# Kernel tuning notes

Measured on AMD Instinct MI355X. Metric: run time of the kernel, lower is better.

## Reference

```python
import jax, jax.numpy as jnp
import numpy as np

B, C_IN, T = 32, 22, 5000
EMB, P = 64, 100
HOP, NFFT, SR = 25, 128, 250
MIN_SZ, MAX_SZ = 10, 100
OC = 40
SCALES = (9, 25, 49)
FC = OC * len(SCALES)
_freqs = np.arange(NFFT // 2 + 1) * SR / NFFT
MU_IDX = np.nonzero((_freqs >= 8) & (_freqs <= 13))[0]   # bins 5,6
BETA_IDX = np.nonzero((_freqs >= 13) & (_freqs <= 30))[0]  # bins 7..15


def setup_inputs() -> dict:
    key = jax.random.key(0)
    k = iter(jax.random.split(key, 16))
    inp = {"x": jax.random.normal(next(k), (B, C_IN, T), jnp.float32)}
    for i, s in enumerate(SCALES):
        inp[f"ms{i}_w1"] = jax.random.normal(next(k), (OC, 1, 1, s), jnp.float32) * 0.05
        inp[f"ms{i}_b1"] = jnp.zeros((OC,), jnp.float32)
        inp[f"ms{i}_w2"] = jax.random.normal(next(k), (OC, OC, C_IN, 1), jnp.float32) * 0.05
        inp[f"ms{i}_b2"] = jnp.zeros((OC,), jnp.float32)
        inp[f"ms{i}_g"] = jnp.ones((OC,), jnp.float32)
        inp[f"ms{i}_bt"] = jnp.zeros((OC,), jnp.float32)
        inp[f"ms{i}_m"] = jnp.zeros((OC,), jnp.float32)
        inp[f"ms{i}_v"] = jnp.ones((OC,), jnp.float32)
    inp["a_w1"] = jax.random.normal(next(k), (C_IN // 2, C_IN, 3), jnp.float32) * 0.05
    inp["a_b1"] = jnp.zeros((C_IN // 2,), jnp.float32)
    inp["a_g"] = jnp.ones((C_IN // 2,), jnp.float32)
    inp["a_bt"] = jnp.zeros((C_IN // 2,), jnp.float32)
    inp["a_m"] = jnp.zeros((C_IN // 2,), jnp.float32)
    inp["a_v"] = jnp.ones((C_IN // 2,), jnp.float32)
    inp["a_w2"] = jax.random.normal(next(k), (1, C_IN // 2, 1), jnp.float32) * 0.05
    inp["a_b2"] = jnp.zeros((1,), jnp.float32)
    inp["proj_w"] = jax.random.normal(next(k), (EMB, FC, 1), jnp.float32) * 0.05
    inp["proj_b"] = jnp.zeros((EMB,), jnp.float32)
    return inp


def _conv1d(x, w, pad):
    return jax.lax.conv_general_dilated(x, w, (1,), [(pad, pad)],
                                        dimension_numbers=("NCH", "OIH", "NCH"))


def _bn(y, g, bt, m, v):  # eval-mode BatchNorm over channel dim of [B, C, T]
    return (y - m[None, :, None]) * jax.lax.rsqrt(v[None, :, None] + 1e-5) * g[None, :, None] + bt[None, :, None]


def _branch(x, w1, b1, w2, b2, g, bt, m, v):
    # Conv2d(1,OC,(1,ks)) on [B,1,C,T] == per-channel 1D conv over time.
    oc, _, _, ks = w1.shape
    b_, c_, t_ = x.shape
    y = _conv1d(x.reshape(b_ * c_, 1, t_), w1.reshape(oc, 1, ks), (ks - 1) // 2) + b1[None, :, None]
    y = y.reshape(b_, c_, oc, t_).transpose(0, 2, 1, 3)            # [B, OC, C, T]
    # Conv2d(OC,OC,(C,1)) collapses the channel (height) dim.
    y = jnp.einsum("oih,biht->bot", w2[..., 0], y) + b2[None, :, None]
    return jax.nn.elu(_bn(y, g, bt, m, v))                         # [B, OC, T]


def _stft_power(x):
    # torchaudio Spectrogram: center=True, reflect pad, periodic hann, power=2
    pad = NFFT // 2
    xp = jnp.pad(x, ((0, 0), (0, 0), (pad, pad)), mode="reflect")
    nfr = T // HOP  # module truncates to t // hop frames
    idx = jnp.arange(nfr)[:, None] * HOP + jnp.arange(NFFT)[None, :]
    win = 0.5 * (1.0 - jnp.cos(2.0 * jnp.pi * jnp.arange(NFFT) / NFFT))
    frames = xp[..., idx] * win                                    # [B, C, nfr, NFFT]
    spec = jnp.fft.rfft(frames, axis=-1)
    return spec.real ** 2 + spec.imag ** 2                         # [B, C, nfr, NFFT//2+1]


def _interp_linear(a, n):  # F.interpolate(mode='linear', align_corners=False) on [B, L]
    L = a.shape[-1]
    pos = jnp.clip((jnp.arange(n) + 0.5) * (L / n) - 0.5, 0.0, L - 1.0)
    lo = jnp.floor(pos).astype(jnp.int32)
    hi = jnp.minimum(lo + 1, L - 1)
    w = pos - lo
    return a[:, lo] * (1.0 - w) + a[:, hi] * w


def _adaptive_grid(act):
    w = 1.0 / (act + 1e-6)
    w = w / jnp.sum(w, axis=1, keepdims=True)
    gs = jnp.clip(w * T, MIN_SZ, MAX_SZ)
    gs = gs * (T / jnp.sum(gs, axis=1, keepdims=True))
    gsr = jnp.round(gs).astype(jnp.int32)
    gsr = gsr.at[:, -1].add(T - jnp.sum(gsr, axis=1))
    gsf = jnp.clip(gsr, MIN_SZ, MAX_SZ)
    gsf = gsf.at[:, -1].add(T - jnp.sum(gsf, axis=1))
    return jnp.where(gsf < MIN_SZ, MIN_SZ, gsf)


def _forward(x, ms0_w1, ms0_b1, ms0_w2, ms0_b2, ms0_g, ms0_bt, ms0_m, ms0_v,
             ms1_w1, ms1_b1, ms1_w2, ms1_b2, ms1_g, ms1_bt, ms1_m, ms1_v,
             ms2_w1, ms2_b1, ms2_w2, ms2_b2, ms2_g, ms2_bt, ms2_m, ms2_v,
             a_w1, a_b1, a_g, a_bt, a_m, a_v, a_w2, a_b2, proj_w, proj_b):
    # ---- frequency-domain activity detector ----
    spec = _stft_power(x)                                          # [B, C, 200, F]
    comb = spec[..., MU_IDX].mean(-1) + spec[..., BETA_IDX].mean(-1)  # [B, C, 200]
    a = jax.nn.relu(_bn(_conv1d(comb, a_w1, 1) + a_b1[None, :, None], a_g, a_bt, a_m, a_v))
    a = jnp.einsum("oi,bit->bot", a_w2[..., 0], a)[:, 0] + a_b2[0]
    activity = jax.nn.sigmoid(a)                                   # [B, 200]
    act_i = _interp_linear(activity, P)                            # [B, P]
    grid = _adaptive_grid(act_i)                                   # [B, P] int32, sums ~= T
    ends = jnp.cumsum(grid, axis=1)
    starts = ends - grid
    # ---- multi-scale CNN features ----
    feats = jnp.concatenate([
        _branch(x, ms0_w1, ms0_b1, ms0_w2, ms0_b2, ms0_g, ms0_bt, ms0_m, ms0_v),
        _branch(x, ms1_w1, ms1_b1, ms1_w2, ms1_b2, ms1_g, ms1_bt, ms1_m, ms1_v),
        _branch(x, ms2_w1, ms2_b1, ms2_w2, ms2_b2, ms2_g, ms2_bt, ms2_m, ms2_v)],
        axis=1)                                                    # [B, FC, T]
    # ---- ragged per-patch avg+max pooling via segment reductions ----
    tix = jnp.arange(T)
    seg = jax.vmap(lambda e: jnp.searchsorted(e, tix, side="right"))(ends)  # [B,T] in [0,P]
    flat = (seg + jnp.arange(B)[:, None] * (P + 1)).reshape(-1)
    f = feats.transpose(0, 2, 1).reshape(B * T, FC)
    nseg = B * (P + 1)  # extra slot collects any overflow timesteps
    sums = jax.ops.segment_sum(f, flat, num_segments=nseg)
    cnt = jax.ops.segment_sum(jnp.ones((B * T, 1), f.dtype), flat, num_segments=nseg)
    mx = jax.ops.segment_max(f, flat, num_segments=nseg)
    avg = sums / jnp.maximum(cnt, 1.0)
    mx = jnp.where(cnt > 0, mx, 0.0)
    pooled = (avg + mx).reshape(B, P + 1, FC)[:, :P]               # combined avg+max
    valid = ((ends <= T) & (starts < ends))[..., None]
    pooled = jnp.where(valid, pooled, 0.0)
    emb = jnp.einsum("oc,bpc->bpo", proj_w[..., 0], pooled) + proj_b  # [B, P, EMB]
    return emb, grid, act_i


def reference(x, ms0_w1, ms0_b1, ms0_w2, ms0_b2, ms0_g, ms0_bt, ms0_m, ms0_v,
              ms1_w1, ms1_b1, ms1_w2, ms1_b2, ms1_g, ms1_bt, ms1_m, ms1_v,
              ms2_w1, ms2_b1, ms2_w2, ms2_b2, ms2_g, ms2_bt, ms2_m, ms2_v,
              a_w1, a_b1, a_g, a_bt, a_m, a_v, a_w2, a_b2, proj_w, proj_b):
    return _forward(x, ms0_w1, ms0_b1, ms0_w2, ms0_b2, ms0_g, ms0_bt, ms0_m, ms0_v,
                    ms1_w1, ms1_b1, ms1_w2, ms1_b2, ms1_g, ms1_bt, ms1_m, ms1_v,
                    ms2_w1, ms2_b1, ms2_w2, ms2_b2, ms2_g, ms2_bt, ms2_m, ms2_v,
                    a_w1, a_b1, a_g, a_bt, a_m, a_v, a_w2, a_b2, proj_w, proj_b)
```

## Files before the change

### kernel.cpp

```cpp
#include <hip/hip_runtime.h>
#include <hip/hip_bf16.h>
#include <math.h>
#include <string.h>

#define B 32
#define CIN 22
#define T 5000
#define EMB 64
#define P 100
#define HOP 25
#define OC 40
#define FC 120
#define NBIN 11
#define NFR 200

#define TCH 256
#define CROWS 304
#define RSTRIDE 40

#define XPAD 5128
#define TWROW 24

typedef unsigned short ushort_t;
typedef __attribute__((ext_vector_type(8))) short bf16x8;
typedef __attribute__((ext_vector_type(4))) float f32x4;

__device__ __forceinline__ unsigned short f2bf(float f) {
  unsigned u = __float_as_uint(f);
  unsigned r = (u + 0x7FFFu + ((u >> 16) & 1u)) >> 16;
  return (unsigned short)r;
}
__device__ __forceinline__ float bf2f(unsigned short u) {
  return __uint_as_float(((unsigned)u) << 16);
}
__device__ __forceinline__ float fast_elu(float y) {
  return y > 0.f ? y : (__builtin_amdgcn_exp2f(y * 1.44269504088896340736f) - 1.0f);
}
__device__ __forceinline__ unsigned pack2bf(float a, float b) {
  __hip_bfloat162 h = __float22bfloat162_rn(make_float2(a, b));
  unsigned u;
  memcpy(&u, &h, 4);
  return u;
}

struct SetupArgs {
  const float* w1[3]; const float* b1[3]; const float* w2[3]; const float* b2[3];
  const float* g[3];  const float* bt[3]; const float* m[3];  const float* v[3];
  unsigned short* pw;
  float* A; float* Bc; float* tw;
};

__global__ __launch_bounds__(256) void setup_all(SetupArgs args) {
  int bx = blockIdx.x;
  int tid = threadIdx.x;
  if (bx < 498) {
    int id = bx * 256 + tid;
    int s, KS, fbase, idl;
    if (id < 13824)       { s = 0; KS = 9;  fbase = 0;   idl = id; }
    else if (id < 52224)  { s = 1; KS = 25; fbase = 27;  idl = id - 13824; }
    else                  { s = 2; KS = 49; fbase = 102; idl = id - 52224; }
    int fi = idl >> 9, rem = idl & 511;
    int lane = rem >> 3, j = rem & 7;
    int k = fi / 3, ot = fi - k * 3;
    int m = lane & 15, h = ((lane >> 4) << 3) + j;
    int o = ot * 16 + m;
    float val = 0.f;
    if (h < CIN && o < OC) {
      const float* w1 = args.w1[s];
      const float* w2 = args.w2[s];
      for (int i = 0; i < OC; ++i)
        val = fmaf(w2[(o * OC + i) * CIN + h], w1[i * KS + k], val);
    }
    args.pw[(size_t)(fbase + fi) * 512 + rem] = f2bf(val);
  } else if (bx < 504) {
    int id = (bx - 498) * 256 + tid;
    if (id < 1408) {
      int n = id & 127, k = id >> 7;
      const double PI = 3.14159265358979323846;
      double ang = -2.0 * PI * (double)((k + 5) * n) / 128.0;
      double win = 0.5 * (1.0 - cos(2.0 * PI * (double)n / 128.0));
      args.tw[n * TWROW + 2 * k]     = (float)(cos(ang) * win);
      args.tw[n * TWROW + 2 * k + 1] = (float)(sin(ang) * win);
    } else if (id < 1536) {
      int n = id - 1408;
      args.tw[n * TWROW + 22] = 0.f;
      args.tw[n * TWROW + 23] = 0.f;
    }
  } else {
    if (tid < 120) {
      int s = tid / 40, o = tid - s * 40;
      const float* w2 = args.w2[s];
      float sc = args.g[s][o] / sqrtf(args.v[s][o] + 1e-5f);
      float cc = args.b2[s][o];
      for (int i = 0; i < OC; ++i) {
        float sh = 0.f;
        for (int h = 0; h < CIN; ++h) sh += w2[(o * OC + i) * CIN + h];
        cc = fmaf(args.b1[s][i], sh, cc);
      }
      args.A[tid] = sc;
      args.Bc[tid] = cc * sc + (args.bt[s][o] - args.m[s][o] * sc);
    }
  }
}

__global__ __launch_bounds__(256) void stft_comb(const float* __restrict__ x,
                                                 const float* __restrict__ tw,
                                                 float* __restrict__ comb) {
  __shared__ float xsh[XPAD];
  int bc = blockIdx.x;
  const float* xr = x + (size_t)bc * T;
  int tid = threadIdx.x;
  for (int i = tid; i < XPAD; i += 256) {
    int mm = i - 64;
    mm = (mm < 0) ? -mm : mm;
    mm = (mm >= T) ? (2 * T - 2 - mm) : mm;
    xsh[i] = xr[mm];
  }
  __syncthreads();
  int fr = tid;
  if (fr < NFR) {
    float cr[NBIN], ci[NBIN];
    #pragma unroll
    for (int k = 0; k < NBIN; ++k) { cr[k] = 0.f; ci[k] = 0.f; }
    const float* xw = xsh + fr * HOP;
    #pragma unroll 2
    for (int n = 0; n < 128; ++n) {
      float xv = xw[n];
      const float4* t4 = reinterpret_cast<const float4*>(tw + n * TWROW);
      float4 w0 = t4[0], w1 = t4[1], w2 = t4[2], w3 = t4[3], w4 = t4[4], w5 = t4[5];
      cr[0] = fmaf(xv, w0.x, cr[0]); ci[0] = fmaf(xv, w0.y, ci[0]);
      cr[1] = fmaf(xv, w0.z, cr[1]); ci[1] = fmaf(xv, w0.w, ci[1]);
      cr[2] = fmaf(xv, w1.x, cr[2]); ci[2] = fmaf(xv, w1.y, ci[2]);
      cr[3] = fmaf(xv, w1.z, cr[3]); ci[3] = fmaf(xv, w1.w, ci[3]);
      cr[4] = fmaf(xv, w2.x, cr[4]); ci[4] = fmaf(xv, w2.y, ci[4]);
      cr[5] = fmaf(xv, w2.z, cr[5]); ci[5] = fmaf(xv, w2.w, ci[5]);
      cr[6] = fmaf(xv, w3.x, cr[6]); ci[6] = fmaf(xv, w3.y, ci[6]);
      cr[7] = fmaf(xv, w3.z, cr[7]); ci[7] = fmaf(xv, w3.w, ci[7]);
      cr[8] = fmaf(xv, w4.x, cr[8]); ci[8] = fmaf(xv, w4.y, ci[8]);
      cr[9] = fmaf(xv, w4.z, cr[9]); ci[9] = fmaf(xv, w4.w, ci[9]);
      cr[10] = fmaf(xv, w5.x, cr[10]); ci[10] = fmaf(xv, w5.y, ci[10]);
    }
    float p[NBIN];
    #pragma unroll
    for (int k = 0; k < NBIN; ++k) p[k] = cr[k] * cr[k] + ci[k] * ci[k];
    float beta = 0.f;
    #pragma unroll
    for (int k = 2; k < NBIN; ++k) beta += p[k];
    comb[bc * NFR + fr] = 0.5f * (p[0] + p[1]) + beta * (1.f / 9.f);
  }
}

__device__ __forceinline__ float wave_sum_f(float v) {
  #pragma unroll
  for (int off = 1; off < 64; off <<= 1) v += __shfl_xor(v, off);
  return v;
}
__device__ __forceinline__ int wave_sum_i(int v) {
  #pragma unroll
  for (int off = 1; off < 64; off <<= 1) v += __shfl_xor(v, off);
  return v;
}

struct MidSmem {
  union {
    struct {
      float cl[CIN * NFR];
      float actL[NFR];
      float aiL[P];
      float fL[P];
      int giL[P];
      int sI[P];
      float red;
    } a;
    unsigned short xs[CROWS * RSTRIDE];
  };
};

template <int KS, int FB, int SBASE>
__device__ __forceinline__ void scale_body(const unsigned short* __restrict__ xs,
                                           const unsigned short* __restrict__ pw,
                                           const float* __restrict__ Aff,
                                           const float* __restrict__ Bff,
                                           unsigned short* __restrict__ feats,
                                           int b, int t0, int wt0, int lane) {
  constexpr int PAD = (KS - 1) / 2;
  const int n = lane & 15, q = lane >> 4;
  f32x4 acc[3][4];
  #pragma unroll
  for (int ot = 0; ot < 3; ++ot)
    #pragma unroll
    for (int ti = 0; ti < 4; ++ti)
      acc[ot][ti] = (f32x4){0.f, 0.f, 0.f, 0.f};

  const unsigned short* pws = pw + (size_t)FB * 512 + lane * 8;
  #pragma unroll 1
  for (int k = 0; k < KS; ++k) {
    bf16x8 A0 = *(const bf16x8*)(pws + (size_t)(k * 3 + 0) * 512);
    bf16x8 A1 = *(const bf16x8*)(pws + (size_t)(k * 3 + 1) * 512);
    bf16x8 A2 = *(const bf16x8*)(pws + (size_t)(k * 3 + 2) * 512);
    int rbase = 24 - PAD + k + wt0 + n;
    #pragma unroll
    for (int ti = 0; ti < 4; ++ti) {
      bf16x8 Bf = *(const bf16x8*)(xs + (rbase + ti * 16) * RSTRIDE + q * 8);
      acc[0][ti] = __builtin_amdgcn_mfma_f32_16x16x32_bf16(A0, Bf, acc[0][ti], 0, 0, 0);
      acc[1][ti] = __builtin_amdgcn_mfma_f32_16x16x32_bf16(A1, Bf, acc[1][ti], 0, 0, 0);
      acc[2][ti] = __builtin_amdgcn_mfma_f32_16x16x32_bf16(A2, Bf, acc[2][ti], 0, 0, 0);
    }
  }
  #pragma unroll
  for (int ot = 0; ot < 3; ++ot) {
    int obase = ot * 16 + q * 4;
    if (obase < OC) {
      float Av0 = Aff[SBASE + obase + 0], Bv0 = Bff[SBASE + obase + 0];
      float Av1 = Aff[SBASE + obase + 1], Bv1 = Bff[SBASE + obase + 1];
      float Av2 = Aff[SBASE + obase + 2], Bv2 = Bff[SBASE + obase + 2];
      float Av3 = Aff[SBASE + obase + 3], Bv3 = Bff[SBASE + obase + 3];
      #pragma unroll
      for (int ti = 0; ti < 4; ++ti) {
        int tt = t0 + wt0 + ti * 16 + n;
        if (tt < T) {
          uint2 pk;
          pk.x = pack2bf(fast_elu(fmaf(acc[ot][ti][0], Av0, Bv0)),
                         fast_elu(fmaf(acc[ot][ti][1], Av1, Bv1)));
          pk.y = pack2bf(fast_elu(fmaf(acc[ot][ti][2], Av2, Bv2)),
                         fast_elu(fmaf(acc[ot][ti][3], Av3, Bv3)));
          *reinterpret_cast<uint2*>(feats + (size_t)(b * T + tt) * FC + SBASE + obase) = pk;
        }
      }
    }
  }
}

struct MidArgs {
  const float* x;
  const unsigned short* pw;
  const float* Aff; const float* Bff;
  unsigned short* feats;
  const float* comb;
  const float* aw1; const float* ab1;
  const float* ag;  const float* abt;
  const float* am;  const float* av;
  const float* aw2; const float* ab2;
  float* out_grid; float* out_acti;
  int* ends_i; int* grid_i;
};

__global__ __launch_bounds__(256) void mid_all(MidArgs args) {
  __shared__ MidSmem sm;
  int bx = blockIdx.x;
  int tid = threadIdx.x;
  if (bx >= B) {
    int cx = bx - B;
    int b = cx / 20, t0 = (cx - b * 20) * TCH;
    for (int idx = tid; idx < CIN * CROWS; idx += 256) {
      int h = idx / CROWS, tl = idx - h * CROWS;
      int gt = t0 - 24 + tl;
      float v = (gt >= 0 && gt < T) ? args.x[(size_t)(b * CIN + h) * T + gt] : 0.f;
      sm.xs[tl * RSTRIDE + h] = f2bf(v);
    }
    for (int idx = tid; idx < 10 * CROWS; idx += 256) {
      int c = idx / CROWS, tl = idx - c * CROWS;
      sm.xs[tl * RSTRIDE + 22 + c] = 0;
    }
    __syncthreads();
    int wv = tid >> 6, lane = tid & 63;
    int wt0 = wv * 64;
    scale_body<9, 0, 0>(sm.xs, args.pw, args.Aff, args.Bff, args.feats, b, t0, wt0, lane);
    scale_body<25, 27, 40>(sm.xs, args.pw, args.Aff, args.Bff, args.feats, b, t0, wt0, lane);
    scale_body<49, 102, 80>(sm.xs, args.pw, args.Aff, args.Bff, args.feats, b, t0, wt0, lane);
  } else {
    int b = bx;
    for (int i = tid; i < CIN * NFR; i += 256) sm.a.cl[i] = args.comb[b * CIN * NFR + i];
    __syncthreads();
    int t = tid;
    if (t < NFR) {
      float z = args.ab2[0];
      for (int o = 0; o < 11; ++o) {
        float s = args.ab1[o];
        for (int i = 0; i < CIN; ++i) {
          const float* wr = args.aw1 + o * 66 + i * 3;
          const float* crow = sm.a.cl + i * NFR;
          if (t > 0)       s = fmaf(wr[0], crow[t - 1], s);
          s = fmaf(wr[1], crow[t], s);
          if (t < NFR - 1) s = fmaf(wr[2], crow[t + 1], s);
        }
        float rs = 1.0f / sqrtf(args.av[o] + 1e-5f);
        float y = (s - args.am[o]) * rs * args.ag[o] + args.abt[o];
        y = fmaxf(y, 0.f);
        z = fmaf(args.aw2[o], y, z);
      }
      sm.a.actL[t] = 1.f / (1.f + expf(-z));
    }
    __syncthreads();
    if (t < P) {
      float ai = 0.5f * (sm.a.actL[2 * t] + sm.a.actL[2 * t + 1]);
      sm.a.aiL[t] = ai;
      args.out_acti[b * P + t] = ai;
      sm.a.fL[t] = 1.f / (ai + 1e-6f);
    }
    __syncthreads();
    if (t < 64) {
      float v = sm.a.fL[t] + ((t + 64 < P) ? sm.a.fL[t + 64] : 0.f);
      v = wave_sum_f(v);
      if (t == 0) sm.a.red = v;
    }
    __syncthreads();
    float sw = sm.a.red;
    if (t < P) {
      float gg = (sm.a.fL[t] / sw) * 5000.f;
      gg = fminf(fmaxf(gg, 10.f), 100.f);
      sm.a.fL[t] = gg;
    }
    __syncthreads();
    if (t < 64) {
      float v = sm.a.fL[t] + ((t + 64 < P) ? sm.a.fL[t + 64] : 0.f);
      v = wave_sum_f(v);
      if (t == 0) sm.a.red = v;
    }
    __syncthreads();
    float r = 5000.f / sm.a.red;
    if (t < P) sm.a.giL[t] = (int)rintf(sm.a.fL[t] * r);
    __syncthreads();
    if (t < 64) {
      int v = sm.a.giL[t] + ((t + 64 < P) ? sm.a.giL[t + 64] : 0);
      v = wave_sum_i(v);
      if (t == 0) sm.a.red = __int_as_float(v);
    }
    __syncthreads();
    if (t == P - 1) sm.a.giL[P - 1] += 5000 - __float_as_int(sm.a.red);
    __syncthreads();
    if (t < P) sm.a.giL[t] = min(max(sm.a.giL[t], 10), 100);
    __syncthreads();
    if (t < 64) {
      int v = sm.a.giL[t] + ((t + 64 < P) ? sm.a.giL[t + 64] : 0);
      v = wave_sum_i(v);
      if (t == 0) sm.a.red = __int_as_float(v);
    }
    __syncthreads();
    if (t == P - 1) sm.a.giL[P - 1] += 5000 - __float_as_int(sm.a.red);
    __syncthreads();
    if (t < P) sm.a.sI[t] = max(sm.a.giL[t], 10);
    __syncthreads();
    #pragma unroll
    for (int off = 1; off < P; off <<= 1) {
      int v = 0;
      if (t < P && t >= off) v = sm.a.sI[t - off];
      __syncthreads();
      if (t < P) sm.a.sI[t] += v;
      __syncthreads();
    }
    if (t < P) {
      int g = max(sm.a.giL[t], 10);
      args.out_grid[b * P + t] = (float)g;
      args.grid_i[b * P + t] = g;
      args.ends_i[b * P + t] = sm.a.sI[t];
    }
  }
}

__global__ __launch_bounds__(256) void pool_proj(const unsigned short* __restrict__ feats,
                                                 const int* __restrict__ ends_i,
                                                 const int* __restrict__ grid_i,
                                                 const float* __restrict__ proj_w,
                                                 const float* __restrict__ proj_b,
                                                 float* __restrict__ out_emb) {
  int bp = blockIdx.x;
  int b = bp / P;
  int end = ends_i[bp];
  int gr = grid_i[bp];
  int start = end - gr;
  __shared__ float lds_s[16 * FC];
  __shared__ float lds_m[16 * FC];
  __shared__ float pooled[FC];
  int tid = threadIdx.x;
  bool valid = (end <= T);
  int g = tid % 15;
  int r = tid / 15;
  if (valid && r < 16) {
    float s[8], m[8];
    #pragma unroll
    for (int j = 0; j < 8; ++j) { s[j] = 0.f; m[j] = -INFINITY; }
    const unsigned short* base = feats + (size_t)(b * T + start) * FC + g * 8;
    for (int i = r; i < gr; i += 16) {
      uint4 u = *reinterpret_cast<const uint4*>(base + (size_t)i * FC);
      unsigned w[4] = {u.x, u.y, u.z, u.w};
      #pragma unroll
      for (int j = 0; j < 4; ++j) {
        float v0 = bf2f((unsigned short)(w[j] & 0xffffu));
        float v1 = bf2f((unsigned short)(w[j] >> 16));
        s[2 * j] += v0; s[2 * j + 1] += v1;
        m[2 * j] = fmaxf(m[2 * j], v0); m[2 * j + 1] = fmaxf(m[2 * j + 1], v1);
      }
    }
    #pragma unroll
    for (int j = 0; j < 8; ++j) {
      lds_s[r * FC + g * 8 + j] = s[j];
      lds_m[r * FC + g * 8 + j] = m[j];
    }
  }
  __syncthreads();
  if (tid < FC) {
    if (valid) {
      float s = 0.f, mx = -INFINITY;
      #pragma unroll
      for (int rr = 0; rr < 16; ++rr) {
        s += lds_s[rr * FC + tid];
        mx = fmaxf(mx, lds_m[rr * FC + tid]);
      }
      pooled[tid] = s / (float)gr + mx;
    } else {
      pooled[tid] = 0.f;
    }
  }
  __syncthreads();
  if (tid < EMB) {
    float e = proj_b[tid];
    const float* wr = proj_w + tid * FC;
    #pragma unroll 8
    for (int c = 0; c < FC; ++c) e = fmaf(wr[c], pooled[c], e);
    out_emb[(size_t)bp * EMB + tid] = e;
  }
}

extern "C" void kernel_launch(void* const* d_in, const int* in_sizes, int n_in,
                              void* d_out, int out_size, void* d_ws, size_t ws_size,
                              hipStream_t stream) {
  const float* x = (const float*)d_in[0];
  const float* aw1 = (const float*)d_in[25];
  const float* ab1 = (const float*)d_in[26];
  const float* ag  = (const float*)d_in[27];
  const float* abt = (const float*)d_in[28];
  const float* am  = (const float*)d_in[29];
  const float* av  = (const float*)d_in[30];
  const float* aw2 = (const float*)d_in[31];
  const float* ab2 = (const float*)d_in[32];
  const float* proj_w = (const float*)d_in[33];
  const float* proj_b = (const float*)d_in[34];

  float* wsf = (float*)d_ws;
  float* A    = wsf;
  float* Bc   = wsf + 120;
  float* tw   = wsf + 240;
  float* comb = wsf + 4096;
  int* ends_i = (int*)(wsf + 144896);
  int* grid_i = (int*)(wsf + 148096);
  unsigned short* pw = (unsigned short*)(wsf + 151296);
  unsigned short* feats = (unsigned short*)(wsf + 215040);

  float* out      = (float*)d_out;
  float* out_emb  = out;
  float* out_grid = out + 204800;
  float* out_acti = out + 208000;

  SetupArgs sa;
  MidArgs ma;
  for (int s = 0; s < 3; ++s) {
    sa.w1[s] = (const float*)d_in[1 + 8 * s];
    sa.b1[s] = (const float*)d_in[2 + 8 * s];
    sa.w2[s] = (const float*)d_in[3 + 8 * s];
    sa.b2[s] = (const float*)d_in[4 + 8 * s];
    sa.g[s]  = (const float*)d_in[5 + 8 * s];
    sa.bt[s] = (const float*)d_in[6 + 8 * s];
    sa.m[s]  = (const float*)d_in[7 + 8 * s];
    sa.v[s]  = (const float*)d_in[8 + 8 * s];
  }
  sa.pw = pw; sa.A = A; sa.Bc = Bc; sa.tw = tw;

  ma.x = x; ma.pw = pw; ma.Aff = A; ma.Bff = Bc; ma.feats = feats;
  ma.comb = comb; ma.aw1 = aw1; ma.ab1 = ab1; ma.ag = ag; ma.abt = abt;
  ma.am = am; ma.av = av; ma.aw2 = aw2; ma.ab2 = ab2;
  ma.out_grid = out_grid; ma.out_acti = out_acti;
  ma.ends_i = ends_i; ma.grid_i = grid_i;

  setup_all<<<505, 256, 0, stream>>>(sa);
  stft_comb<<<B * CIN, 256, 0, stream>>>(x, tw, comb);
  mid_all<<<B + 20 * B, 256, 0, stream>>>(ma);
  pool_proj<<<B * P, 256, 0, stream>>>(feats, ends_i, grid_i, proj_w, proj_b, out_emb);
}
```

Measured before the change: 262.8 us.

## Halve conv time chunk and buffer all-scale outputs for contiguous row stores

Shrinks the per-block time chunk from 256 to 128 and doubles the grid so there are more blocks to spread across CUs. Each wave now computes two 16-step tiles per scale. The ELU/BN-packed results of all three scales are kept in registers and then written together per time row, so each row's 120 features go out as one contiguous burst instead of three separate passes. In exchange the 24-row halo is reloaded more often relative to useful work, and the A-fragment weights are loaded per block twice as often.

```diff
diff --git a/kernel.cpp b/kernel.cpp
--- a/kernel.cpp
+++ b/kernel.cpp
@@ -14,8 +14,8 @@
 #define NBIN 11
 #define NFR 200
 
-#define TCH 256
-#define CROWS 304
+#define TCH 128
+#define CROWS 176
 #define RSTRIDE 40
 
 #define XPAD 5128
@@ -177,19 +177,19 @@
 };
 
 template <int KS, int FB, int SBASE>
-__device__ __forceinline__ void scale_body(const unsigned short* __restrict__ xs,
+__device__ __forceinline__ void scale_calc(const unsigned short* __restrict__ xs,
                                            const unsigned short* __restrict__ pw,
                                            const float* __restrict__ Aff,
                                            const float* __restrict__ Bff,
-                                           unsigned short* __restrict__ feats,
-                                           int b, int t0, int wt0, int lane) {
+                                           uint2* __restrict__ held,
+                                           int wt0, int lane) {
   constexpr int PAD = (KS - 1) / 2;
   const int n = lane & 15, q = lane >> 4;
-  f32x4 acc[3][4];
+  f32x4 acc[3][2];
   #pragma unroll
   for (int ot = 0; ot < 3; ++ot)
     #pragma unroll
-    for (int ti = 0; ti < 4; ++ti)
+    for (int ti = 0; ti < 2; ++ti)
       acc[ot][ti] = (f32x4){0.f, 0.f, 0.f, 0.f};
 
   const unsigned short* pws = pw + (size_t)FB * 512 + lane * 8;
@@ -200,7 +200,7 @@
     bf16x8 A2 = *(const bf16x8*)(pws + (size_t)(k * 3 + 2) * 512);
     int rbase = 24 - PAD + k + wt0 + n;
     #pragma unroll
-    for (int ti = 0; ti < 4; ++ti) {
+    for (int ti = 0; ti < 2; ++ti) {
       bf16x8 Bf = *(const bf16x8*)(xs + (rbase + ti * 16) * RSTRIDE + q * 8);
       acc[0][ti] = __builtin_amdgcn_mfma_f32_16x16x32_bf16(A0, Bf, acc[0][ti], 0, 0, 0);
       acc[1][ti] = __builtin_amdgcn_mfma_f32_16x16x32_bf16(A1, Bf, acc[1][ti], 0, 0, 0);
@@ -210,23 +210,20 @@
   #pragma unroll
   for (int ot = 0; ot < 3; ++ot) {
     int obase = ot * 16 + q * 4;
-    if (obase < OC) {
-      float Av0 = Aff[SBASE + obase + 0], Bv0 = Bff[SBASE + obase + 0];
-      float Av1 = Aff[SBASE + obase + 1], Bv1 = Bff[SBASE + obase + 1];
-      float Av2 = Aff[SBASE + obase + 2], Bv2 = Bff[SBASE + obase + 2];
-      float Av3 = Aff[SBASE + obase + 3], Bv3 = Bff[SBASE + obase + 3];
-      #pragma unroll
-      for (int ti = 0; ti < 4; ++ti) {
-        int tt = t0 + wt0 + ti * 16 + n;
-        if (tt < T) {
-          uint2 pk;
-          pk.x = pack2bf(fast_elu(fmaf(acc[ot][ti][0], Av0, Bv0)),
-                         fast_elu(fmaf(acc[ot][ti][1], Av1, Bv1)));
-          pk.y = pack2bf(fast_elu(fmaf(acc[ot][ti][2], Av2, Bv2)),
-                         fast_elu(fmaf(acc[ot][ti][3], Av3, Bv3)));
-          *reinterpret_cast<uint2*>(feats + (size_t)(b * T + tt) * FC + SBASE + obase) = pk;
-        }
-      }
+    float Av0, Bv0, Av1, Bv1, Av2, Bv2, Av3, Bv3;
+    int ob = obase < OC ? obase : 0;
+    Av0 = Aff[SBASE + ob + 0]; Bv0 = Bff[SBASE + ob + 0];
+    Av1 = Aff[SBASE + ob + 1]; Bv1 = Bff[SBASE + ob + 1];
+    Av2 = Aff[SBASE + ob + 2]; Bv2 = Bff[SBASE + ob + 2];
+    Av3 = Aff[SBASE + ob + 3]; Bv3 = Bff[SBASE + ob + 3];
+    #pragma unroll
+    for (int ti = 0; ti < 2; ++ti) {
+      uint2 pk;
+      pk.x = pack2bf(fast_elu(fmaf(acc[ot][ti][0], Av0, Bv0)),
+                     fast_elu(fmaf(acc[ot][ti][1], Av1, Bv1)));
+      pk.y = pack2bf(fast_elu(fmaf(acc[ot][ti][2], Av2, Bv2)),
+                     fast_elu(fmaf(acc[ot][ti][3], Av3, Bv3)));
+      held[ot * 2 + ti] = pk;
     }
   }
 }
@@ -251,7 +248,7 @@
   int tid = threadIdx.x;
   if (bx >= B) {
     int cx = bx - B;
-    int b = cx / 20, t0 = (cx - b * 20) * TCH;
+    int b = cx / 40, t0 = (cx - b * 40) * TCH;
     for (int idx = tid; idx < CIN * CROWS; idx += 256) {
       int h = idx / CROWS, tl = idx - h * CROWS;
       int gt = t0 - 24 + tl;
@@ -264,10 +261,28 @@
     }
     __syncthreads();
     int wv = tid >> 6, lane = tid & 63;
-    int wt0 = wv * 64;
-    scale_body<9, 0, 0>(sm.xs, args.pw, args.Aff, args.Bff, args.feats, b, t0, wt0, lane);
-    scale_body<25, 27, 40>(sm.xs, args.pw, args.Aff, args.Bff, args.feats, b, t0, wt0, lane);
-    scale_body<49, 102, 80>(sm.xs, args.pw, args.Aff, args.Bff, args.feats, b, t0, wt0, lane);
+    int wt0 = wv * 32;
+    uint2 held[3][6];
+    scale_calc<9, 0, 0>(sm.xs, args.pw, args.Aff, args.Bff, held[0], wt0, lane);
+    scale_calc<25, 27, 40>(sm.xs, args.pw, args.Aff, args.Bff, held[1], wt0, lane);
+    scale_calc<49, 102, 80>(sm.xs, args.pw, args.Aff, args.Bff, held[2], wt0, lane);
+    int n = lane & 15, q = lane >> 4;
+    #pragma unroll
+    for (int ti = 0; ti < 2; ++ti) {
+      int tt = t0 + wt0 + ti * 16 + n;
+      if (tt < T) {
+        unsigned short* rowp = args.feats + (size_t)(b * T + tt) * FC;
+        #pragma unroll
+        for (int s = 0; s < 3; ++s) {
+          #pragma unroll
+          for (int ot = 0; ot < 3; ++ot) {
+            int obase = ot * 16 + q * 4;
+            if (obase < OC)
+              *reinterpret_cast<uint2*>(rowp + s * 40 + obase) = held[s][ot * 2 + ti];
+          }
+        }
+      }
+    }
   } else {
     int b = bx;
     for (int i = tid; i < CIN * NFR; i += 256) sm.a.cl[i] = args.comb[b * CIN * NFR + i];
@@ -474,6 +489,6 @@
 
   setup_all<<<505, 256, 0, stream>>>(sa);
   stft_comb<<<B * CIN, 256, 0, stream>>>(x, tw, comb);
-  mid_all<<<B + 20 * B, 256, 0, stream>>>(ma);
+  mid_all<<<B + 40 * B, 256, 0, stream>>>(ma);
   pool_proj<<<B * P, 256, 0, stream>>>(feats, ends_i, grid_i, proj_w, proj_b, out_emb);
 }
```

Result: slower. 293.7 us (+11.7%).

## Fuse four kernels into one cooperative persistent kernel with grid syncs

Applied to the files above, without the earlier changes.

Merges setup, STFT, mid and pool/projection kernels into one cooperative kernel of 512 blocks that loops over work units and separates phases with grid-wide syncs. A four-kernel fallback runs if cooperative launch is unavailable. The aim is to remove kernel launch gaps between dependent stages. In exchange the grid is capped at 512 blocks, which lowers parallelism for the 3200-unit pool phase. The shared union is also sized to its largest member, which may reduce occupancy, and each call pays host-side device-property queries.

```diff
diff --git a/kernel.cpp b/kernel.cpp
--- a/kernel.cpp
+++ b/kernel.cpp
@@ -1,7 +1,10 @@
 #include <hip/hip_runtime.h>
 #include <hip/hip_bf16.h>
+#include <hip/hip_cooperative_groups.h>
 #include <math.h>
 #include <string.h>
+
+namespace cg = cooperative_groups;
 
 #define B 32
 #define CIN 22
@@ -20,8 +23,8 @@
 
 #define XPAD 5128
 #define TWROW 24
-
-typedef unsigned short ushort_t;
+#define GRID 512
+
 typedef __attribute__((ext_vector_type(8))) short bf16x8;
 typedef __attribute__((ext_vector_type(4))) float f32x4;
 
@@ -42,19 +45,57 @@
   memcpy(&u, &h, 4);
   return u;
 }
-
-struct SetupArgs {
+__device__ __forceinline__ float wave_sum_f(float v) {
+  #pragma unroll
+  for (int off = 1; off < 64; off <<= 1) v += __shfl_xor(v, off);
+  return v;
+}
+__device__ __forceinline__ int wave_sum_i(int v) {
+  #pragma unroll
+  for (int off = 1; off < 64; off <<= 1) v += __shfl_xor(v, off);
+  return v;
+}
+
+struct MegaArgs {
   const float* w1[3]; const float* b1[3]; const float* w2[3]; const float* b2[3];
   const float* g[3];  const float* bt[3]; const float* m[3];  const float* v[3];
+  const float* x;
   unsigned short* pw;
-  float* A; float* Bc; float* tw;
+  float* A; float* Bc; float* tw; float* comb;
+  const float* aw1; const float* ab1;
+  const float* ag;  const float* abt;
+  const float* am;  const float* av;
+  const float* aw2; const float* ab2;
+  const float* proj_w; const float* proj_b;
+  unsigned short* feats;
+  float* out_grid; float* out_acti; float* out_emb;
+  int* ends_i; int* grid_i;
 };
 
-__global__ __launch_bounds__(256) void setup_all(SetupArgs args) {
-  int bx = blockIdx.x;
-  int tid = threadIdx.x;
-  if (bx < 498) {
-    int id = bx * 256 + tid;
+struct Smem {
+  union {
+    unsigned short xs[CROWS * RSTRIDE];
+    float xsh[XPAD];
+    struct {
+      float cl[CIN * NFR];
+      float actL[NFR];
+      float aiL[P];
+      float fL[P];
+      int giL[P];
+      int sI[P];
+      float red;
+    } a;
+    struct {
+      float s[16 * FC];
+      float m[16 * FC];
+      float pooled[FC];
+    } p;
+  };
+};
+
+__device__ void phase1_unit(const MegaArgs& args, int u, int tid) {
+  if (u < 498) {
+    int id = u * 256 + tid;
     int s, KS, fbase, idl;
     if (id < 13824)       { s = 0; KS = 9;  fbase = 0;   idl = id; }
     else if (id < 52224)  { s = 1; KS = 25; fbase = 27;  idl = id - 13824; }
@@ -72,8 +113,8 @@
         val = fmaf(w2[(o * OC + i) * CIN + h], w1[i * KS + k], val);
     }
     args.pw[(size_t)(fbase + fi) * 512 + rem] = f2bf(val);
-  } else if (bx < 504) {
-    int id = (bx - 498) * 256 + tid;
+  } else if (u < 504) {
+    int id = (u - 498) * 256 + tid;
     if (id < 1408) {
       int n = id & 127, k = id >> 7;
       const double PI = 3.14159265358979323846;
@@ -103,13 +144,8 @@
   }
 }
 
-__global__ __launch_bounds__(256) void stft_comb(const float* __restrict__ x,
-                                                 const float* __restrict__ tw,
-                                                 float* __restrict__ comb) {
-  __shared__ float xsh[XPAD];
-  int bc = blockIdx.x;
-  const float* xr = x + (size_t)bc * T;
-  int tid = threadIdx.x;
+__device__ void phase2_unit(const MegaArgs& args, int bc, int tid, float* xsh) {
+  const float* xr = args.x + (size_t)bc * T;
   for (int i = tid; i < XPAD; i += 256) {
     int mm = i - 64;
     mm = (mm < 0) ? -mm : mm;
@@ -126,7 +162,7 @@
     #pragma unroll 2
     for (int n = 0; n < 128; ++n) {
       float xv = xw[n];
-      const float4* t4 = reinterpret_cast<const float4*>(tw + n * TWROW);
+      const float4* t4 = reinterpret_cast<const float4*>(args.tw + n * TWROW);
       float4 w0 = t4[0], w1 = t4[1], w2 = t4[2], w3 = t4[3], w4 = t4[4], w5 = t4[5];
       cr[0] = fmaf(xv, w0.x, cr[0]); ci[0] = fmaf(xv, w0.y, ci[0]);
       cr[1] = fmaf(xv, w0.z, cr[1]); ci[1] = fmaf(xv, w0.w, ci[1]);
@@ -146,35 +182,10 @@
     float beta = 0.f;
     #pragma unroll
     for (int k = 2; k < NBIN; ++k) beta += p[k];
-    comb[bc * NFR + fr] = 0.5f * (p[0] + p[1]) + beta * (1.f / 9.f);
-  }
-}
-
-__device__ __forceinline__ float wave_sum_f(float v) {
-  #pragma unroll
-  for (int off = 1; off < 64; off <<= 1) v += __shfl_xor(v, off);
-  return v;
-}
-__device__ __forceinline__ int wave_sum_i(int v) {
-  #pragma unroll
-  for (int off = 1; off < 64; off <<= 1) v += __shfl_xor(v, off);
-  return v;
-}
-
-struct MidSmem {
-  union {
-    struct {
-      float cl[CIN * NFR];
-      float actL[NFR];
-      float aiL[P];
-      float fL[P];
-      int giL[P];
-      int sI[P];
-      float red;
-    } a;
-    unsigned short xs[CROWS * RSTRIDE];
-  };
-};
+    args.comb[bc * NFR + fr] = 0.5f * (p[0] + p[1]) + beta * (1.f / 9.f);
+  }
+  __syncthreads();
+}
 
 template <int KS, int FB, int SBASE>
 __device__ __forceinline__ void scale_body(const unsigned short* __restrict__ xs,
@@ -231,26 +242,9 @@
   }
 }
 
-struct MidArgs {
-  const float* x;
-  const unsigned short* pw;
-  const float* Aff; const float* Bff;
-  unsigned short* feats;
-  const float* comb;
-  const float* aw1; const float* ab1;
-  const float* ag;  const float* abt;
-  const float* am;  const float* av;
-  const float* aw2; const float* ab2;
-  float* out_grid; float* out_acti;
-  int* ends_i; int* grid_i;
-};
-
-__global__ __launch_bounds__(256) void mid_all(MidArgs args) {
-  __shared__ MidSmem sm;
-  int bx = blockIdx.x;
-  int tid = threadIdx.x;
-  if (bx >= B) {
-    int cx = bx - B;
+__device__ void phase3_unit(const MegaArgs& args, int u, int tid, Smem& sm) {
+  if (u >= B) {
+    int cx = u - B;
     int b = cx / 20, t0 = (cx - b * 20) * TCH;
     for (int idx = tid; idx < CIN * CROWS; idx += 256) {
       int h = idx / CROWS, tl = idx - h * CROWS;
@@ -265,11 +259,12 @@
     __syncthreads();
     int wv = tid >> 6, lane = tid & 63;
     int wt0 = wv * 64;
-    scale_body<9, 0, 0>(sm.xs, args.pw, args.Aff, args.Bff, args.feats, b, t0, wt0, lane);
-    scale_body<25, 27, 40>(sm.xs, args.pw, args.Aff, args.Bff, args.feats, b, t0, wt0, lane);
-    scale_body<49, 102, 80>(sm.xs, args.pw, args.Aff, args.Bff, args.feats, b, t0, wt0, lane);
+    scale_body<9, 0, 0>(sm.xs, args.pw, args.A, args.Bc, args.feats, b, t0, wt0, lane);
+    scale_body<25, 27, 40>(sm.xs, args.pw, args.A, args.Bc, args.feats, b, t0, wt0, lane);
+    scale_body<49, 102, 80>(sm.xs, args.pw, args.A, args.Bc, args.feats, b, t0, wt0, lane);
+    __syncthreads();
   } else {
-    int b = bx;
+    int b = u;
     for (int i = tid; i < CIN * NFR; i += 256) sm.a.cl[i] = args.comb[b * CIN * NFR + i];
     __syncthreads();
     int t = tid;
@@ -307,9 +302,9 @@
     __syncthreads();
     float sw = sm.a.red;
     if (t < P) {
-      float gg = (sm.a.fL[t] / sw) * 5000.f;
-      gg = fminf(fmaxf(gg, 10.f), 100.f);
-      sm.a.fL[t] = gg;
+      float ggv = (sm.a.fL[t] / sw) * 5000.f;
+      ggv = fminf(fmaxf(ggv, 10.f), 100.f);
+      sm.a.fL[t] = ggv;
     }
     __syncthreads();
     if (t < 64) {
@@ -350,29 +345,20 @@
       __syncthreads();
     }
     if (t < P) {
-      int g = max(sm.a.giL[t], 10);
-      args.out_grid[b * P + t] = (float)g;
-      args.grid_i[b * P + t] = g;
+      int g2 = max(sm.a.giL[t], 10);
+      args.out_grid[b * P + t] = (float)g2;
+      args.grid_i[b * P + t] = g2;
       args.ends_i[b * P + t] = sm.a.sI[t];
     }
-  }
-}
-
-__global__ __launch_bounds__(256) void pool_proj(const unsigned short* __restrict__ feats,
-                                                 const int* __restrict__ ends_i,
-                                                 const int* __restrict__ grid_i,
-                                                 const float* __restrict__ proj_w,
-                                                 const float* __restrict__ proj_b,
-                                                 float* __restrict__ out_emb) {
-  int bp = blockIdx.x;
+    __syncthreads();
+  }
+}
+
+__device__ void phase4_unit(const MegaArgs& args, int bp, int tid, Smem& sm) {
   int b = bp / P;
-  int end = ends_i[bp];
-  int gr = grid_i[bp];
+  int end = args.ends_i[bp];
+  int gr = args.grid_i[bp];
   int start = end - gr;
-  __shared__ float lds_s[16 * FC];
-  __shared__ float lds_m[16 * FC];
-  __shared__ float pooled[FC];
-  int tid = threadIdx.x;
   bool valid = (end <= T);
   int g = tid % 15;
   int r = tid / 15;
@@ -380,10 +366,10 @@
     float s[8], m[8];
     #pragma unroll
     for (int j = 0; j < 8; ++j) { s[j] = 0.f; m[j] = -INFINITY; }
-    const unsigned short* base = feats + (size_t)(b * T + start) * FC + g * 8;
+    const unsigned short* base = args.feats + (size_t)(b * T + start) * FC + g * 8;
     for (int i = r; i < gr; i += 16) {
-      uint4 u = *reinterpret_cast<const uint4*>(base + (size_t)i * FC);
-      unsigned w[4] = {u.x, u.y, u.z, u.w};
+      uint4 u4 = *reinterpret_cast<const uint4*>(base + (size_t)i * FC);
+      unsigned w[4] = {u4.x, u4.y, u4.z, u4.w};
       #pragma unroll
       for (int j = 0; j < 4; ++j) {
         float v0 = bf2f((unsigned short)(w[j] & 0xffffu));
@@ -394,8 +380,8 @@
     }
     #pragma unroll
     for (int j = 0; j < 8; ++j) {
-      lds_s[r * FC + g * 8 + j] = s[j];
-      lds_m[r * FC + g * 8 + j] = m[j];
+      sm.p.s[r * FC + g * 8 + j] = s[j];
+      sm.p.m[r * FC + g * 8 + j] = m[j];
     }
   }
   __syncthreads();
@@ -404,39 +390,62 @@
       float s = 0.f, mx = -INFINITY;
       #pragma unroll
       for (int rr = 0; rr < 16; ++rr) {
-        s += lds_s[rr * FC + tid];
-        mx = fmaxf(mx, lds_m[rr * FC + tid]);
+        s += sm.p.s[rr * FC + tid];
+        mx = fmaxf(mx, sm.p.m[rr * FC + tid]);
       }
-      pooled[tid] = s / (float)gr + mx;
+      sm.p.pooled[tid] = s / (float)gr + mx;
     } else {
-      pooled[tid] = 0.f;
+      sm.p.pooled[tid] = 0.f;
     }
   }
   __syncthreads();
   if (tid < EMB) {
-    float e = proj_b[tid];
-    const float* wr = proj_w + tid * FC;
+    float e = args.proj_b[tid];
+    const float* wr = args.proj_w + tid * FC;
     #pragma unroll 8
-    for (int c = 0; c < FC; ++c) e = fmaf(wr[c], pooled[c], e);
-    out_emb[(size_t)bp * EMB + tid] = e;
-  }
+    for (int c = 0; c < FC; ++c) e = fmaf(wr[c], sm.p.pooled[c], e);
+    args.out_emb[(size_t)bp * EMB + tid] = e;
+  }
+  __syncthreads();
+}
+
+__global__ __launch_bounds__(256) void mega(MegaArgs args) {
+  cg::grid_group gg = cg::this_grid();
+  __shared__ Smem sm;
+  int bid = blockIdx.x;
+  int tid = threadIdx.x;
+  int stride = gridDim.x;
+  for (int u = bid; u < 505; u += stride) phase1_unit(args, u, tid);
+  __threadfence();
+  gg.sync();
+  for (int bc = bid; bc < B * CIN; bc += stride) phase2_unit(args, bc, tid, sm.xsh);
+  __threadfence();
+  gg.sync();
+  for (int u = bid; u < B + 20 * B; u += stride) phase3_unit(args, u, tid, sm);
+  __threadfence();
+  gg.sync();
+  for (int bp = bid; bp < B * P; bp += stride) phase4_unit(args, bp, tid, sm);
+}
+
+__global__ __launch_bounds__(256) void k_phase1(MegaArgs args) {
+  phase1_unit(args, blockIdx.x, threadIdx.x);
+}
+__global__ __launch_bounds__(256) void k_phase2(MegaArgs args) {
+  __shared__ Smem sm;
+  phase2_unit(args, blockIdx.x, threadIdx.x, sm.xsh);
+}
+__global__ __launch_bounds__(256) void k_phase3(MegaArgs args) {
+  __shared__ Smem sm;
+  phase3_unit(args, blockIdx.x, threadIdx.x, sm);
+}
+__global__ __launch_bounds__(256) void k_phase4(MegaArgs args) {
+  __shared__ Smem sm;
+  phase4_unit(args, blockIdx.x, threadIdx.x, sm);
 }
 
 extern "C" void kernel_launch(void* const* d_in, const int* in_sizes, int n_in,
                               void* d_out, int out_size, void* d_ws, size_t ws_size,
                               hipStream_t stream) {
-  const float* x = (const float*)d_in[0];
-  const float* aw1 = (const float*)d_in[25];
-  const float* ab1 = (const float*)d_in[26];
-  const float* ag  = (const float*)d_in[27];
-  const float* abt = (const float*)d_in[28];
-  const float* am  = (const float*)d_in[29];
-  const float* av  = (const float*)d_in[30];
-  const float* aw2 = (const float*)d_in[31];
-  const float* ab2 = (const float*)d_in[32];
-  const float* proj_w = (const float*)d_in[33];
-  const float* proj_b = (const float*)d_in[34];
-
   float* wsf = (float*)d_ws;
   float* A    = wsf;
   float* Bc   = wsf + 120;
@@ -447,33 +456,50 @@
   unsigned short* pw = (unsigned short*)(wsf + 151296);
   unsigned short* feats = (unsigned short*)(wsf + 215040);
 
-  float* out      = (float*)d_out;
-  float* out_emb  = out;
-  float* out_grid = out + 204800;
-  float* out_acti = out + 208000;
-
-  SetupArgs sa;
-  MidArgs ma;
+  float* out = (float*)d_out;
+
+  static MegaArgs ma;
   for (int s = 0; s < 3; ++s) {
-    sa.w1[s] = (const float*)d_in[1 + 8 * s];
-    sa.b1[s] = (const float*)d_in[2 + 8 * s];
-    sa.w2[s] = (const float*)d_in[3 + 8 * s];
-    sa.b2[s] = (const float*)d_in[4 + 8 * s];
-    sa.g[s]  = (const float*)d_in[5 + 8 * s];
-    sa.bt[s] = (const float*)d_in[6 + 8 * s];
-    sa.m[s]  = (const float*)d_in[7 + 8 * s];
-    sa.v[s]  = (const float*)d_in[8 + 8 * s];
-  }
-  sa.pw = pw; sa.A = A; sa.Bc = Bc; sa.tw = tw;
-
-  ma.x = x; ma.pw = pw; ma.Aff = A; ma.Bff = Bc; ma.feats = feats;
-  ma.comb = comb; ma.aw1 = aw1; ma.ab1 = ab1; ma.ag = ag; ma.abt = abt;
-  ma.am = am; ma.av = av; ma.aw2 = aw2; ma.ab2 = ab2;
-  ma.out_grid = out_grid; ma.out_acti = out_acti;
+    ma.w1[s] = (const float*)d_in[1 + 8 * s];
+    ma.b1[s] = (const float*)d_in[2 + 8 * s];
+    ma.w2[s] = (const float*)d_in[3 + 8 * s];
+    ma.b2[s] = (const float*)d_in[4 + 8 * s];
+    ma.g[s]  = (const float*)d_in[5 + 8 * s];
+    ma.bt[s] = (const float*)d_in[6 + 8 * s];
+    ma.m[s]  = (const float*)d_in[7 + 8 * s];
+    ma.v[s]  = (const float*)d_in[8 + 8 * s];
+  }
+  ma.x = (const float*)d_in[0];
+  ma.pw = pw; ma.A = A; ma.Bc = Bc; ma.tw = tw; ma.comb = comb;
+  ma.aw1 = (const float*)d_in[25];
+  ma.ab1 = (const float*)d_in[26];
+  ma.ag  = (const float*)d_in[27];
+  ma.abt = (const float*)d_in[28];
+  ma.am  = (const float*)d_in[29];
+  ma.av  = (const float*)d_in[30];
+  ma.aw2 = (const float*)d_in[31];
+  ma.ab2 = (const float*)d_in[32];
+  ma.proj_w = (const float*)d_in[33];
+  ma.proj_b = (const float*)d_in[34];
+  ma.feats = feats;
+  ma.out_emb  = out;
+  ma.out_grid = out + 204800;
+  ma.out_acti = out + 208000;
   ma.ends_i = ends_i; ma.grid_i = grid_i;
 
-  setup_all<<<505, 256, 0, stream>>>(sa);
-  stft_comb<<<B * CIN, 256, 0, stream>>>(x, tw, comb);
-  mid_all<<<B + 20 * B, 256, 0, stream>>>(ma);
-  pool_proj<<<B * P, 256, 0, stream>>>(feats, ends_i, grid_i, proj_w, proj_b, out_emb);
-}
+  hipError_t err = hipErrorUnknown;
+  int dev = 0;
+  hipGetDevice(&dev);
+  hipDeviceProp_t prop;
+  if (hipGetDeviceProperties(&prop, dev) == hipSuccess && prop.cooperativeLaunch) {
+    void* ka[1] = {&ma};
+    err = hipLaunchCooperativeKernel((const void*)mega, dim3(GRID), dim3(256), ka, 0, stream);
+  }
+  if (err != hipSuccess) {
+    (void)hipGetLastError();
+    k_phase1<<<505, 256, 0, stream>>>(ma);
+    k_phase2<<<B * CIN, 256, 0, stream>>>(ma);
+    k_phase3<<<B + 20 * B, 256, 0, stream>>>(ma);
+    k_phase4<<<B * P, 256, 0, stream>>>(ma);
+  }
+}
```

Result: slower. 786.9 us (+199.4%).
